# Optimization experiments

Hardware: AMD Instinct MI355X
Metric: run time of the kernel (lower is better)

Reference implementation:

```python
import jax, jax.numpy as jnp
import numpy as np

STRIDES = (8, 16, 32, 64, 128)
LEVEL_HW = ((128, 160), (64, 80), (32, 40), (16, 20), (8, 10))
IMG_H, IMG_W = 1024, 1280
B, NUM_CLASSES = 16, 20
SCORE_THR, IOU_THR, MAX_DET = 0.05, 0.6, 1000


def _coords_all():
    # coords_fmap2orig for every level, concatenated -> [N, 2] (x, y)
    cs = []
    for (h, w), s in zip(LEVEL_HW, STRIDES):
        sx = jnp.arange(w, dtype=jnp.float32) * s + s // 2
        sy = jnp.arange(h, dtype=jnp.float32) * s + s // 2
        yy, xx = jnp.meshgrid(sy, sx, indexing='ij')
        cs.append(jnp.stack([xx.reshape(-1), yy.reshape(-1)], -1))
    return jnp.concatenate(cs, 0)


def _reshape_cat(levels):
    # list of [B,C,h,w] -> [B, sum(h*w), C]
    return jnp.concatenate(
        [p.transpose(0, 2, 3, 1).reshape(p.shape[0], -1, p.shape[1]) for p in levels], 1)


def _decode(cls_l, cnt_l, reg_l, coords):
    cls = jax.nn.sigmoid(_reshape_cat(cls_l))           # [B,N,C]
    cnt = jax.nn.sigmoid(_reshape_cat(cnt_l))[..., 0]   # [B,N]
    reg = _reshape_cat(reg_l)                           # [B,N,4] ltrb
    scores = jnp.sqrt(jnp.max(cls, -1) * cnt)           # add_centerness + sqrt
    classes = jnp.argmax(cls, -1) + 1
    boxes = jnp.concatenate([coords[None] - reg[..., :2], coords[None] + reg[..., 2:]], -1)
    return scores, classes, boxes


def _nms_keep(boxes, scores, classes, valid):
    # masked greedy per-class NMS on fixed size M; returns keep mask [M]
    boxes = jax.lax.stop_gradient(boxes)
    scores = jax.lax.stop_gradient(scores)
    maxc = jnp.max(jnp.where(valid[:, None], boxes, 0.0))
    b = boxes + (classes.astype(boxes.dtype) * (maxc + 1.0))[:, None]  # class offsets
    order = jnp.argsort(-jnp.where(valid, scores, -jnp.inf))
    b = b[order]
    v = valid[order]
    x1, y1, x2, y2 = b[:, 0], b[:, 1], b[:, 2], b[:, 3]
    areas = (x2 - x1 + 1.0) * (y2 - y1 + 1.0)
    iw = jnp.clip(jnp.minimum(x2[:, None], x2[None, :]) - jnp.maximum(x1[:, None], x1[None, :]) + 1.0, 0.0)
    ih = jnp.clip(jnp.minimum(y2[:, None], y2[None, :]) - jnp.maximum(y1[:, None], y1[None, :]) + 1.0, 0.0)
    inter = iw * ih
    iou = inter / (areas[:, None] + areas[None, :] - inter)
    M = boxes.shape[0]

    def body(i, carry):
        keep, sup = carry
        k = v[i] & (~sup[i])
        keep = keep.at[i].set(k)
        sup = sup | (k & (iou[i] > IOU_THR))
        return keep, sup

    keep_s, _ = jax.lax.fori_loop(0, M, body, (jnp.zeros(M, bool), jnp.zeros(M, bool)))
    return jnp.zeros(M, bool).at[order].set(keep_s)


def _forward(args):
    cls_r, cnt_r, reg_r = args[0:5], args[5:10], args[10:15]
    cls_i, cnt_i, reg_i = args[15:20], args[20:25], args[25:30]
    coords = _coords_all()
    s_r, c_r, b_r = _decode(cls_r, cnt_r, reg_r, coords)
    s_i, c_i, b_i = _decode(cls_i, cnt_i, reg_i, coords)
    scores = jnp.concatenate([s_r, s_i], 1)   # [B, 2N]
    classes = jnp.concatenate([c_r, c_i], 1)
    boxes = jnp.concatenate([b_r, b_i], 1)
    top_s, top_i = jax.lax.top_k(scores, MAX_DET)
    top_c = jnp.take_along_axis(classes, top_i, 1)
    top_b = jnp.take_along_axis(boxes, top_i[..., None], 1)
    valid = top_s >= SCORE_THR
    keep = jax.vmap(_nms_keep)(top_b, top_s, top_c, valid)
    # ClipBoxes: clamp to image bounds
    top_b = jnp.maximum(top_b, 0.0)
    xs = jnp.minimum(top_b[..., 0::2], IMG_W - 1.0)
    ys = jnp.minimum(top_b[..., 1::2], IMG_H - 1.0)
    top_b = jnp.stack([xs[..., 0], ys[..., 0], xs[..., 1], ys[..., 1]], -1)
    kf = keep.astype(top_s.dtype)
    return top_s * kf, top_c * keep, top_b * kf[..., None], keep


def setup_inputs() -> dict:
    key = jax.random.key(0)
    chans = {'cls': NUM_CLASSES, 'cnt': 1, 'reg': 4}
    inp = {}
    i = 0
    for mod in ('r', 'i'):
        for kind in ('cls', 'cnt', 'reg'):
            for l, (h, w) in enumerate(LEVEL_HW):
                k = jax.random.fold_in(key, i); i += 1
                inp[f'{kind}_{mod}_{l}'] = jax.random.normal(k, (B, chans[kind], h, w), jnp.float32)
    return inp


def reference(cls_r_0, cls_r_1, cls_r_2, cls_r_3, cls_r_4,
              cnt_r_0, cnt_r_1, cnt_r_2, cnt_r_3, cnt_r_4,
              reg_r_0, reg_r_1, reg_r_2, reg_r_3, reg_r_4,
              cls_i_0, cls_i_1, cls_i_2, cls_i_3, cls_i_4,
              cnt_i_0, cnt_i_1, cnt_i_2, cnt_i_3, cnt_i_4,
              reg_i_0, reg_i_1, reg_i_2, reg_i_3, reg_i_4):
    args = [cls_r_0, cls_r_1, cls_r_2, cls_r_3, cls_r_4,
            cnt_r_0, cnt_r_1, cnt_r_2, cnt_r_3, cnt_r_4,
            reg_r_0, reg_r_1, reg_r_2, reg_r_3, reg_r_4,
            cls_i_0, cls_i_1, cls_i_2, cls_i_3, cls_i_4,
            cnt_i_0, cnt_i_1, cnt_i_2, cnt_i_3, cnt_i_4,
            reg_i_0, reg_i_1, reg_i_2, reg_i_3, reg_i_4]
    return _forward(args)
```

## Files before the change

### kernel.cpp

```cpp
#include <hip/hip_runtime.h>
#include <hip/hip_bf16.h>

typedef unsigned long long u64;
typedef unsigned int u32;

#define NTOT    54560
#define NMOD    27280
#define BATCH   16
#define KPAD    1024
#define MAXD    1000
#define NBIN    16384
#define CANDCAP 6144

struct Ptrs { const float* p[30]; };

constexpr size_t SZ_KEY   = (size_t)BATCH * NTOT * 8;
constexpr size_t SZ_TOPK  = (size_t)BATCH * KPAD * 8;
constexpr size_t SZ_TRAW  = (size_t)BATCH * KPAD * 16;
constexpr size_t SZ_T1    = (size_t)BATCH * KPAD * 4;
constexpr size_t SZ_MAXC  = (size_t)BATCH * 32 * 4;
constexpr size_t SZ_VALID = (size_t)BATCH * 32 * 4;
constexpr size_t SZ_MASK  = (size_t)BATCH * KPAD * 32 * 4;

constexpr size_t OFF_KEY    = 0;
constexpr size_t OFF_TOPK   = OFF_KEY   + SZ_KEY;
constexpr size_t OFF_TRAW   = OFF_TOPK  + SZ_TOPK;
constexpr size_t OFF_TSCORE = OFF_TRAW  + SZ_TRAW;
constexpr size_t OFF_TCLSF  = OFF_TSCORE+ SZ_T1;
constexpr size_t OFF_MAXC   = OFF_TCLSF + SZ_T1;
constexpr size_t OFF_VALID  = OFF_MAXC  + SZ_MAXC;
constexpr size_t OFF_MASK   = OFF_VALID + SZ_VALID;

__device__ inline void level_of(int nm, int& l, int& pos, int& w, int& s, int& hw) {
    if (nm < 20480)      { l = 0; pos = nm;         w = 160; s = 8;   hw = 20480; }
    else if (nm < 25600) { l = 1; pos = nm - 20480; w = 80;  s = 16;  hw = 5120; }
    else if (nm < 26880) { l = 2; pos = nm - 25600; w = 40;  s = 32;  hw = 1280; }
    else if (nm < 27200) { l = 3; pos = nm - 26880; w = 20;  s = 64;  hw = 320; }
    else                 { l = 4; pos = nm - 27200; w = 10;  s = 128; hw = 80; }
}

__device__ inline float sigm(float x) { return 1.0f / (1.0f + expf(-x)); }

__global__ __launch_bounds__(256) __attribute__((amdgpu_waves_per_eu(2, 4)))
void decode_kernel(Ptrs ptrs, u64* __restrict__ keyAll) {
    int t = blockIdx.x * 256 + threadIdx.x;
    int b = blockIdx.y;
    if (t >= NTOT) return;
    int q = t & 3;
    int n0 = t & ~3;
    int mod = (n0 >= NMOD) ? 1 : 0;
    int nm = n0 - mod * NMOD;
    int l, pos, w, s, hw;
    level_of(nm, l, pos, w, s, hw);
    (void)w; (void)s;
    const float* clsP = ptrs.p[mod * 15 + l];
    const float* cntP = ptrs.p[mod * 15 + 5 + l];
    const float4* cb = (const float4*)(clsP + (size_t)b * 20 * hw + pos);
    int hw4 = hw >> 2;
    int c0 = q * 5;
    float4 v[5];
    #pragma unroll
    for (int c = 0; c < 5; ++c) v[c] = cb[(size_t)(c0 + c) * hw4];
    float4 cv = *(const float4*)(cntP + (size_t)b * hw + pos);

    float4 mx = v[0];
    #pragma unroll
    for (int c = 1; c < 5; ++c) {
        mx.x = fmaxf(mx.x, v[c].x); mx.y = fmaxf(mx.y, v[c].y);
        mx.z = fmaxf(mx.z, v[c].z); mx.w = fmaxf(mx.w, v[c].w);
    }
    mx.x = fmaxf(mx.x, __shfl_xor(mx.x, 1));
    mx.y = fmaxf(mx.y, __shfl_xor(mx.y, 1));
    mx.z = fmaxf(mx.z, __shfl_xor(mx.z, 1));
    mx.w = fmaxf(mx.w, __shfl_xor(mx.w, 1));
    mx.x = fmaxf(mx.x, __shfl_xor(mx.x, 2));
    mx.y = fmaxf(mx.y, __shfl_xor(mx.y, 2));
    mx.z = fmaxf(mx.z, __shfl_xor(mx.z, 2));
    mx.w = fmaxf(mx.w, __shfl_xor(mx.w, 2));

    float ma = (q & 1) ? ((q & 2) ? mx.w : mx.y) : ((q & 2) ? mx.z : mx.x);
    float ca = (q & 1) ? ((q & 2) ? cv.w : cv.y) : ((q & 2) ? cv.z : cv.x);
    u32 sb = __float_as_uint(sqrtf(__fmul_rn(sigm(ma), sigm(ca))));
    keyAll[(size_t)b * NTOT + t] = ((u64)sb << 16) | (u64)(65535 - t);
}

__global__ __launch_bounds__(1024)
void select_kernel(const u64* __restrict__ keyAll, u64* __restrict__ topkey,
                   u32* __restrict__ maxcG) {
    int b = blockIdx.x, tid = threadIdx.x;
    int lane = tid & 63, wid = tid >> 6;
    __shared__ u32 shist[NBIN];
    __shared__ u32 warep[16];
    __shared__ int sB1;
    __shared__ u32 scnt;
    double* sd = (double*)shist;

    if (tid == 0) { maxcG[b * 32] = 0u; scnt = 0u; }
    #pragma unroll
    for (int j = 0; j < NBIN / 1024; ++j) shist[tid + j * 1024] = 0u;
    __syncthreads();

    const u64* keys = keyAll + (size_t)b * NTOT;
    const u64 SENT = ~0ull;
    for (int n0 = 0; n0 < NTOT; n0 += 8192) {
        u64 kk[8];
        #pragma unroll
        for (int r = 0; r < 8; ++r) {
            int idx = n0 + r * 1024 + tid;
            kk[r] = (idx < NTOT) ? keys[idx] : SENT;
        }
        #pragma unroll
        for (int r = 0; r < 8; ++r)
            if (kk[r] != SENT) atomicAdd(&shist[(u32)(kk[r] >> 32)], 1u);
    }
    __syncthreads();

    u32 loc[16]; u32 sum = 0;
    #pragma unroll
    for (int j = 0; j < 16; ++j) { loc[j] = shist[NBIN - 1 - (tid * 16 + j)]; sum += loc[j]; }
    u32 v = sum;
    #pragma unroll
    for (int off = 1; off < 64; off <<= 1) {
        u32 t2 = (u32)__shfl_up((int)v, off);
        if (lane >= off) v += t2;
    }
    if (lane == 63) warep[wid] = v;
    __syncthreads();
    if (tid < 16) {
        u32 p = warep[tid];
        #pragma unroll
        for (int off = 1; off < 16; off <<= 1) {
            u32 t2 = (u32)__shfl_up((int)p, off);
            if (tid >= off) p += t2;
        }
        warep[tid] = p;
    }
    __syncthreads();
    u32 incl = v + (wid ? warep[wid - 1] : 0u);
    u32 excl = incl - sum;
    if (excl < (u32)MAXD && incl >= (u32)MAXD) {
        u32 c = excl;
        #pragma unroll
        for (int j = 0; j < 16; ++j) {
            c += loc[j];
            if (c >= (u32)MAXD) { sB1 = NBIN - 1 - (tid * 16 + j); break; }
        }
    }
    __syncthreads();
    int B1 = sB1;

    for (int n0 = 0; n0 < NTOT; n0 += 8192) {
        u64 kk[8];
        #pragma unroll
        for (int r = 0; r < 8; ++r) {
            int idx = n0 + r * 1024 + tid;
            kk[r] = (idx < NTOT) ? keys[idx] : 0ull;
        }
        #pragma unroll
        for (int r = 0; r < 8; ++r) {
            if (kk[r] != 0ull && (int)(kk[r] >> 32) >= B1) {
                u32 p = atomicAdd(&scnt, 1u);
                if (p < CANDCAP - 2) sd[p] = (double)kk[r];
            }
        }
    }
    __syncthreads();
    int C = min((int)scnt, CANDCAP - 2);
    if (tid == 0) { sd[C] = -1.0; sd[C + 1] = -1.0; }
    __syncthreads();

    for (int i = tid; i < C; i += 1024) {
        double ki = sd[i];
        int rank = 0;
        const double2* sd2 = (const double2*)sd;
        int C2 = (C + 1) >> 1;
        for (int j = 0; j < C2; ++j) {
            double2 v2 = sd2[j];
            rank += (v2.x > ki) ? 1 : 0;
            rank += (v2.y > ki) ? 1 : 0;
        }
        if (rank < MAXD) topkey[(size_t)b * KPAD + rank] = (u64)ki;
    }
}

__global__ __launch_bounds__(128) __attribute__((amdgpu_waves_per_eu(2, 4)))
void gather_kernel(Ptrs ptrs, const u64* __restrict__ topkey,
                   float4* __restrict__ traw, float* __restrict__ tscore,
                   float* __restrict__ tclsf, u32* __restrict__ validwords,
                   u32* __restrict__ maxcG) {
    #pragma clang fp contract(off)
    int b = blockIdx.y;
    int tid = threadIdx.x;
    int half = tid & 1;
    int i = blockIdx.x * 64 + (tid >> 1);
    int active = (i < MAXD);

    float score = 0.f;
    float best = -1.0f; int bi = 0;
    float ra = 0.f, rb2 = 0.f;
    int pos = 0, w = 1, s = 0;
    if (active) {
        u64 key = topkey[(size_t)b * KPAD + i];
        int n = 65535 - (int)(key & 0xFFFFull);
        score = __uint_as_float((u32)(key >> 16));
        int mod = (n >= NMOD) ? 1 : 0;
        int nm = n - mod * NMOD;
        int l, hw;
        level_of(nm, l, pos, w, s, hw);
        const float* clsP = ptrs.p[mod * 15 + l];
        const float* regP = ptrs.p[mod * 15 + 10 + l];
        const float* cbp = clsP + (size_t)b * 20 * hw + pos;
        const float* rbp = regP + (size_t)b * 4 * hw + pos;
        float cl[10];
        int c0 = half * 10;
        #pragma unroll
        for (int c = 0; c < 10; ++c) cl[c] = cbp[(size_t)(c0 + c) * hw];
        ra  = rbp[(size_t)(half * 2) * hw];
        rb2 = rbp[(size_t)(half * 2 + 1) * hw];
        #pragma unroll
        for (int c = 0; c < 10; ++c) {
            float p = sigm(cl[c]);
            if (p > best) { best = p; bi = c0 + c; }
        }
    }
    float po  = __shfl_xor(best, 1);
    int   bio = __shfl_xor(bi, 1);
    float rao = __shfl_xor(ra, 1);
    float rbo = __shfl_xor(rb2, 1);
    if (half == 0) { if (po > best)  { best = po; bi = bio; } }
    else           { if (po >= best) { best = po; bi = bio; } }
    float clsf = active ? (float)(bi + 1) : 0.f;
    float r0 = half ? rao : ra,  r1 = half ? rbo : rb2;
    float r2 = half ? ra  : rao, r3 = half ? rb2 : rbo;

    float4 bx = make_float4(0.f, 0.f, 0.f, 0.f);
    if (active) {
        int xi = pos % w, yi = pos / w;
        float cx = (float)(xi * s + (s >> 1));
        float cy = (float)(yi * s + (s >> 1));
        bx.x = cx - r0; bx.y = cy - r1; bx.z = cx + r2; bx.w = cy + r3;
    }
    int valid = active && (score >= 0.05f) && (half == 0);
    float contrib = valid ? fmaxf(0.0f, fmaxf(fmaxf(bx.x, bx.y), fmaxf(bx.z, bx.w))) : 0.0f;
    float red = contrib;
    #pragma unroll
    for (int off = 32; off > 0; off >>= 1) red = fmaxf(red, __shfl_down(red, off));
    if ((tid & 63) == 0) atomicMax(&maxcG[b * 32], __float_as_uint(red));
    u64 ball = __ballot(valid != 0);
    if ((tid & 63) == 0) {
        u32 word = 0;
        for (int j = 0; j < 32; ++j) word |= (u32)((ball >> (2 * j)) & 1ull) << j;
        validwords[b * 32 + blockIdx.x * 2 + (tid >> 6)] = word;
    }
    if (half == 0) {
        size_t oo = (size_t)b * KPAD + i;
        traw[oo] = bx; tscore[oo] = score; tclsf[oo] = clsf;
    }
}

#define SW(t) ((((t) & 31) << 3) | ((t) >> 5))
__global__ __launch_bounds__(64)
void mask_kernel(const float4* __restrict__ traw, const float* __restrict__ tclsf,
                 const u32* __restrict__ maxcG, u32* __restrict__ maskG) {
    #pragma clang fp contract(off)
    int u = blockIdx.x, b = blockIdx.y, tid = threadIdx.x;
    int g, wg;
    if (u < 128)      { g = u >> 2;                 wg = u & 3; }
    else if (u < 224) { int i2 = u - 128; g = 32 + i2 / 3;      wg = 1 + i2 % 3; }
    else if (u < 288) { int i2 = u - 224; g = 64 + (i2 >> 1);   wg = 2 + (i2 & 1); }
    else              { g = 96 + (u - 288);         wg = 3; }
    int i0 = g * 8, j0 = wg * 256;
    float m1 = __uint_as_float(maxcG[b * 32]) + 1.0f;

    __shared__ float cx1[256], cy1[256], cx2[256], cy2[256], ca[256];
    for (int t = tid; t < 256; t += 64) {
        float4 f = traw[(size_t)b * KPAD + j0 + t];
        float o = __fmul_rn(tclsf[(size_t)b * KPAD + j0 + t], m1);
        float ox1 = __fadd_rn(f.x, o), oy1 = __fadd_rn(f.y, o);
        float ox2 = __fadd_rn(f.z, o), oy2 = __fadd_rn(f.w, o);
        float dw = ox2 - ox1 + 1.0f;
        float dh = oy2 - oy1 + 1.0f;
        int ts = SW(t);
        cx1[ts] = ox1; cy1[ts] = oy1; cx2[ts] = ox2; cy2[ts] = oy2;
        ca[ts] = __fmul_rn(dw, dh);
    }
    __syncthreads();

    int ir = tid >> 3, wr = tid & 7;
    int i = i0 + ir;
    float4 fi = traw[(size_t)b * KPAD + i];
    float oi = __fmul_rn(tclsf[(size_t)b * KPAD + i], m1);
    float ix1 = __fadd_rn(fi.x, oi), iy1 = __fadd_rn(fi.y, oi);
    float ix2 = __fadd_rn(fi.z, oi), iy2 = __fadd_rn(fi.w, oi);
    float dwi = ix2 - ix1 + 1.0f, dhi = iy2 - iy1 + 1.0f;
    float ai = __fmul_rn(dwi, dhi);
    u32 bits = 0;
    int jb = wr * 32;
    for (int jj = 0; jj < 32; ++jj) {
        int js = SW(jb + jj);
        float iw = fminf(ix2, cx2[js]) - fmaxf(ix1, cx1[js]) + 1.0f;
        iw = fmaxf(iw, 0.0f);
        float ih = fminf(iy2, cy2[js]) - fmaxf(iy1, cy1[js]) + 1.0f;
        ih = fmaxf(ih, 0.0f);
        float inter = iw * ih;
        float denom = (ai + ca[js]) - inter;
        float iou = inter / denom;
        bits |= (iou > 0.6f) ? (1u << jj) : 0u;
    }
    maskG[((size_t)b * KPAD + i) * 32 + wg * 8 + wr] = bits;
}

__global__ __launch_bounds__(64)
void scan_out_kernel(const u32* __restrict__ maskG, const u32* __restrict__ validbits,
                     const float4* __restrict__ traw, const float* __restrict__ tscore,
                     const float* __restrict__ tclsf, float* __restrict__ out) {
    int b = blockIdx.x, lane = threadIdx.x;
    int lw = lane & 31;
    const u32* mrow = maskG + (size_t)b * KPAD * 32;
    u32 vreg = (lane < 32) ? validbits[b * 32 + lane] : 0u;
    u32 removed = 0u, keepw = 0u;
    u32 mA[8], mB[8];
    #pragma unroll
    for (int d = 0; d < 8; ++d) {
        mA[d] = mrow[(size_t)d * 32 + lw];
        mB[d] = mrow[(size_t)(d + 8) * 32 + lw];
    }
    auto step8 = [&](int base, u32* ms) {
        #pragma unroll
        for (int d = 0; d < 8; ++d) {
            int i = base + d;
            int wi = i >> 5, bi2 = i & 31;
            u32 rw = (u32)__builtin_amdgcn_readlane((int)removed, wi);
            u32 vw = (u32)__builtin_amdgcn_readlane((int)vreg, wi);
            u32 k = ((vw >> bi2) & 1u) & (~(rw >> bi2) & 1u);
            if (k) removed |= ms[d];
            if (lane == wi) keepw |= (k << bi2);
            ms[d] = mrow[(size_t)(i + 16) * 32 + lw];
        }
    };
    for (int t = 0; t < 62; ++t) { step8(t * 16, mA); step8(t * 16 + 8, mB); }
    step8(992, mA);

    __shared__ u32 keeps[32];
    if (lane < 32) keeps[lane] = keepw;
    __syncthreads();
    const int BQ = BATCH * MAXD;
    for (int s2 = lane; s2 < MAXD; s2 += 64) {
        u32 kf = (keeps[s2 >> 5] >> (s2 & 31)) & 1u;
        size_t oo = (size_t)b * KPAD + s2;
        float score = tscore[oo];
        float clsf = tclsf[oo];
        float4 bx = traw[oo];
        float x1 = fminf(fmaxf(bx.x, 0.f), 1279.f);
        float y1 = fminf(fmaxf(bx.y, 0.f), 1023.f);
        float x2 = fminf(fmaxf(bx.z, 0.f), 1279.f);
        float y2 = fminf(fmaxf(bx.w, 0.f), 1023.f);
        int base = b * MAXD + s2;
        out[base] = kf ? score : 0.0f;
        out[BQ + base] = kf ? clsf : 0.0f;
        float* ob = out + 2 * BQ + (size_t)base * 4;
        ob[0] = kf ? x1 : 0.f; ob[1] = kf ? y1 : 0.f;
        ob[2] = kf ? x2 : 0.f; ob[3] = kf ? y2 : 0.f;
        out[6 * BQ + base] = kf ? 1.0f : 0.0f;
    }
}

extern "C" void kernel_launch(void* const* d_in, const int* in_sizes, int n_in,
                              void* d_out, int out_size, void* d_ws, size_t ws_size,
                              hipStream_t stream) {
    Ptrs ptrs;
    for (int i = 0; i < 30; ++i) ptrs.p[i] = (const float*)d_in[i];

    char* ws = (char*)d_ws;
    u64*    keyAll    = (u64*)   (ws + OFF_KEY);
    u64*    topkey    = (u64*)   (ws + OFF_TOPK);
    float4* traw      = (float4*)(ws + OFF_TRAW);
    float*  tscore    = (float*) (ws + OFF_TSCORE);
    float*  tclsf     = (float*) (ws + OFF_TCLSF);
    u32*    maxcG     = (u32*)   (ws + OFF_MAXC);
    u32*    validbits = (u32*)   (ws + OFF_VALID);
    u32*    maskG     = (u32*)   (ws + OFF_MASK);
    float*  out       = (float*)d_out;

    decode_kernel<<<dim3((NTOT + 255) / 256, BATCH), 256, 0, stream>>>(ptrs, keyAll);
    select_kernel<<<BATCH, 1024, 0, stream>>>(keyAll, topkey, maxcG);
    gather_kernel<<<dim3(16, BATCH), 128, 0, stream>>>(ptrs, topkey, traw, tscore, tclsf,
                                                       validbits, maxcG);
    mask_kernel<<<dim3(320, BATCH), 64, 0, stream>>>(traw, tclsf, maxcG, maskG);
    scan_out_kernel<<<BATCH, 64, 0, stream>>>(maskG, validbits, traw, tscore, tclsf, out);
}
```

Before: 284.3 us.

## Stage decode inputs via global_load_lds and preload NMS mask into LDS

Result: faster. 277.6 us (-2.4%).

```diff
diff --git a/kernel.cpp b/kernel.cpp
--- a/kernel.cpp
+++ b/kernel.cpp
@@ -11,6 +11,7 @@
 #define MAXD    1000
 #define NBIN    16384
 #define CANDCAP 6144
+#define NLDSPOS 25600
 
 struct Ptrs { const float* p[30]; };
 
@@ -41,15 +42,68 @@
 
 __device__ inline float sigm(float x) { return 1.0f / (1.0f + expf(-x)); }
 
-__global__ __launch_bounds__(256) __attribute__((amdgpu_waves_per_eu(2, 4)))
-void decode_kernel(Ptrs ptrs, u64* __restrict__ keyAll) {
+__device__ inline void ld_lds16(const float* g, float* l) {
+    __builtin_amdgcn_global_load_lds(
+        (const __attribute__((address_space(1))) void*)g,
+        (__attribute__((address_space(3))) void*)l, 16, 0, 0);
+}
+
+__global__ __launch_bounds__(256)
+void decode_lds_kernel(Ptrs ptrs, u64* __restrict__ keyAll) {
+    __shared__ float lds[21 * 1024];
+    int cc = blockIdx.x;
+    int b = blockIdx.y;
+    int mod = cc / 25, c = cc % 25;
+    int l     = (c < 20) ? 0 : 1;
+    int hw    = (c < 20) ? 20480 : 5120;
+    int pos0  = (c < 20) ? c * 1024 : (c - 20) * 1024;
+    int nmb   = (l == 0) ? pos0 : 20480 + pos0;
+    const float* clsP = ptrs.p[mod * 15 + l];
+    const float* cntP = ptrs.p[mod * 15 + 5 + l];
+    int wave = threadIdx.x >> 6, lane = threadIdx.x & 63;
+
+    const float* cbase = clsP + (size_t)b * 20 * hw + pos0 + wave * 256 + lane * 4;
+    float* dbase = lds + wave * 256;
+    #pragma unroll
+    for (int ch = 0; ch < 20; ++ch)
+        ld_lds16(cbase + (size_t)ch * hw, dbase + ch * 1024);
+    ld_lds16(cntP + (size_t)b * hw + pos0 + wave * 256 + lane * 4, dbase + 20 * 1024);
+    __syncthreads();
+
+    int t = threadIdx.x;
+    const float4* l4 = (const float4*)lds;
+    float4 mx = l4[t];
+    #pragma unroll
+    for (int ch = 1; ch < 20; ++ch) {
+        float4 v = l4[ch * 256 + t];
+        mx.x = fmaxf(mx.x, v.x); mx.y = fmaxf(mx.y, v.y);
+        mx.z = fmaxf(mx.z, v.z); mx.w = fmaxf(mx.w, v.w);
+    }
+    float4 cv = l4[20 * 256 + t];
+
+    int n = mod * NMOD + nmb + t * 4;
+    u32 s0 = __float_as_uint(sqrtf(__fmul_rn(sigm(mx.x), sigm(cv.x))));
+    u32 s1 = __float_as_uint(sqrtf(__fmul_rn(sigm(mx.y), sigm(cv.y))));
+    u32 s2 = __float_as_uint(sqrtf(__fmul_rn(sigm(mx.z), sigm(cv.z))));
+    u32 s3 = __float_as_uint(sqrtf(__fmul_rn(sigm(mx.w), sigm(cv.w))));
+    ulonglong2* ka2 = (ulonglong2*)(keyAll + (size_t)b * NTOT + n);
+    ulonglong2 k01, k23;
+    k01.x = ((u64)s0 << 16) | (u64)(65535 - n);
+    k01.y = ((u64)s1 << 16) | (u64)(65535 - (n + 1));
+    k23.x = ((u64)s2 << 16) | (u64)(65535 - (n + 2));
+    k23.y = ((u64)s3 << 16) | (u64)(65535 - (n + 3));
+    ka2[0] = k01; ka2[1] = k23;
+}
+
+__global__ __launch_bounds__(256)
+void decode_tail_kernel(Ptrs ptrs, u64* __restrict__ keyAll) {
     int t = blockIdx.x * 256 + threadIdx.x;
     int b = blockIdx.y;
-    if (t >= NTOT) return;
+    if (t >= 3360) return;
+    int mod = t / 1680;
+    int tm = t % 1680;
     int q = t & 3;
-    int n0 = t & ~3;
-    int mod = (n0 >= NMOD) ? 1 : 0;
-    int nm = n0 - mod * NMOD;
+    int nm = 25600 + (tm & ~3);
     int l, pos, w, s, hw;
     level_of(nm, l, pos, w, s, hw);
     (void)w; (void)s;
@@ -81,7 +135,8 @@
     float ma = (q & 1) ? ((q & 2) ? mx.w : mx.y) : ((q & 2) ? mx.z : mx.x);
     float ca = (q & 1) ? ((q & 2) ? cv.w : cv.y) : ((q & 2) ? cv.z : cv.x);
     u32 sb = __float_as_uint(sqrtf(__fmul_rn(sigm(ma), sigm(ca))));
-    keyAll[(size_t)b * NTOT + t] = ((u64)sb << 16) | (u64)(65535 - t);
+    int n = mod * NMOD + nm + q;
+    keyAll[(size_t)b * NTOT + n] = ((u64)sb << 16) | (u64)(65535 - n);
 }
 
 __global__ __launch_bounds__(1024)
@@ -183,7 +238,7 @@
     }
 }
 
-__global__ __launch_bounds__(128) __attribute__((amdgpu_waves_per_eu(2, 4)))
+__global__ __launch_bounds__(128)
 void gather_kernel(Ptrs ptrs, const u64* __restrict__ topkey,
                    float4* __restrict__ traw, float* __restrict__ tscore,
                    float* __restrict__ tclsf, u32* __restrict__ validwords,
@@ -310,42 +365,51 @@
     maskG[((size_t)b * KPAD + i) * 32 + wg * 8 + wr] = bits;
 }
 
-__global__ __launch_bounds__(64)
+__global__ __launch_bounds__(512)
 void scan_out_kernel(const u32* __restrict__ maskG, const u32* __restrict__ validbits,
                      const float4* __restrict__ traw, const float* __restrict__ tscore,
                      const float* __restrict__ tclsf, float* __restrict__ out) {
-    int b = blockIdx.x, lane = threadIdx.x;
-    int lw = lane & 31;
-    const u32* mrow = maskG + (size_t)b * KPAD * 32;
-    u32 vreg = (lane < 32) ? validbits[b * 32 + lane] : 0u;
-    u32 removed = 0u, keepw = 0u;
-    u32 mA[8], mB[8];
-    #pragma unroll
-    for (int d = 0; d < 8; ++d) {
-        mA[d] = mrow[(size_t)d * 32 + lw];
-        mB[d] = mrow[(size_t)(d + 8) * 32 + lw];
-    }
-    auto step8 = [&](int base, u32* ms) {
+    __shared__ u32 sm[KPAD * 32];
+    __shared__ u32 keeps[32];
+    int b = blockIdx.x, tid = threadIdx.x;
+
+    const uint4* s4 = (const uint4*)(maskG + (size_t)b * KPAD * 32);
+    uint4* d4 = (uint4*)sm;
+    #pragma unroll
+    for (int r = 0; r < 16; ++r) d4[tid + r * 512] = s4[tid + r * 512];
+    __syncthreads();
+
+    if (tid < 64) {
+        int lane = tid, lw = lane & 31;
+        u32 vreg = (lane < 32) ? validbits[b * 32 + lane] : 0u;
+        u32 removed = 0u, keepw = 0u;
+        u32 mA[8], mB[8];
         #pragma unroll
         for (int d = 0; d < 8; ++d) {
-            int i = base + d;
-            int wi = i >> 5, bi2 = i & 31;
-            u32 rw = (u32)__builtin_amdgcn_readlane((int)removed, wi);
-            u32 vw = (u32)__builtin_amdgcn_readlane((int)vreg, wi);
-            u32 k = ((vw >> bi2) & 1u) & (~(rw >> bi2) & 1u);
-            if (k) removed |= ms[d];
-            if (lane == wi) keepw |= (k << bi2);
-            ms[d] = mrow[(size_t)(i + 16) * 32 + lw];
-        }
-    };
-    for (int t = 0; t < 62; ++t) { step8(t * 16, mA); step8(t * 16 + 8, mB); }
-    step8(992, mA);
-
-    __shared__ u32 keeps[32];
-    if (lane < 32) keeps[lane] = keepw;
-    __syncthreads();
+            mA[d] = sm[d * 32 + lw];
+            mB[d] = sm[(d + 8) * 32 + lw];
+        }
+        auto step8 = [&](int base, u32* ms) {
+            #pragma unroll
+            for (int d = 0; d < 8; ++d) {
+                int i = base + d;
+                int wi = i >> 5, bi2 = i & 31;
+                u32 rw = (u32)__builtin_amdgcn_readlane((int)removed, wi);
+                u32 vw = (u32)__builtin_amdgcn_readlane((int)vreg, wi);
+                u32 k = ((vw >> bi2) & 1u) & (~(rw >> bi2) & 1u);
+                if (k) removed |= ms[d];
+                if (lane == wi) keepw |= (k << bi2);
+                ms[d] = sm[(i + 16) * 32 + lw];
+            }
+        };
+        for (int t = 0; t < 62; ++t) { step8(t * 16, mA); step8(t * 16 + 8, mB); }
+        step8(992, mA);
+        if (lane < 32) keeps[lane] = keepw;
+    }
+    __syncthreads();
+
     const int BQ = BATCH * MAXD;
-    for (int s2 = lane; s2 < MAXD; s2 += 64) {
+    for (int s2 = tid; s2 < MAXD; s2 += 512) {
         u32 kf = (keeps[s2 >> 5] >> (s2 & 31)) & 1u;
         size_t oo = (size_t)b * KPAD + s2;
         float score = tscore[oo];
@@ -382,10 +446,11 @@
     u32*    maskG     = (u32*)   (ws + OFF_MASK);
     float*  out       = (float*)d_out;
 
-    decode_kernel<<<dim3((NTOT + 255) / 256, BATCH), 256, 0, stream>>>(ptrs, keyAll);
+    decode_lds_kernel<<<dim3(50, BATCH), 256, 0, stream>>>(ptrs, keyAll);
+    decode_tail_kernel<<<dim3(14, BATCH), 256, 0, stream>>>(ptrs, keyAll);
     select_kernel<<<BATCH, 1024, 0, stream>>>(keyAll, topkey, maxcG);
     gather_kernel<<<dim3(16, BATCH), 128, 0, stream>>>(ptrs, topkey, traw, tscore, tclsf,
                                                        validbits, maxcG);
     mask_kernel<<<dim3(320, BATCH), 64, 0, stream>>>(traw, tclsf, maxcG, maskG);
-    scan_out_kernel<<<BATCH, 64, 0, stream>>>(maskG, validbits, traw, tscore, tclsf, out);
-}
+    scan_out_kernel<<<BATCH, 512, 0, stream>>>(maskG, validbits, traw, tscore, tclsf, out);
+}
```
